# Optimization experiments

Hardware: AMD Instinct MI355X
Metric: run time of the kernel (lower is better)

Reference implementation:

```python
import jax, jax.numpy as jnp
import numpy as np

NEG_SLOPE = 0.2  # PyG GATConv default leaky_relu slope


def _gat_layer(h, mask, W, att_src, att_dst, bias, concat):
    """PyG-style GATConv (eval mode, add_self_loops handled via mask diag).
    h: [B,N,D_in], mask: [B,N,N] bool (mask[b,i,j]=True if edge j->i, incl. self loop)
    W: [D_in, H*C], att_src/att_dst: [H,C], bias: [H*C] or [C].
    """
    B, N, _ = h.shape
    H, C = att_src.shape
    x = (h @ W).reshape(B, N, H, C)                       # [B,N,H,C]
    e_src = jnp.einsum('bnhc,hc->bnh', x, att_src)        # score contrib of source j
    e_dst = jnp.einsum('bnhc,hc->bnh', x, att_dst)        # score contrib of target i
    # scores[b,i,j,h] = leaky_relu(e_dst_i + e_src_j)
    s = jax.nn.leaky_relu(e_dst[:, :, None, :] + e_src[:, None, :, :], NEG_SLOPE)
    s = jnp.where(mask[..., None], s, -jnp.inf)
    alpha = jax.nn.softmax(s, axis=2)                     # softmax over neighbors j
    out = jnp.einsum('bijh,bjhc->bihc', alpha, x)         # aggregate
    out = out.reshape(B, N, H * C) if concat else out.mean(axis=2)
    return out + bias


def setup_inputs() -> dict:
    key = jax.random.key(0)
    ks = jax.random.split(key, 16)
    B, T, N, F_in = 4, 8, 2000, 158
    D, H = 128, 4
    C = D // H  # 32
    x_alpha = jax.random.normal(ks[0], (B, T, N, F_in), dtype=jnp.float32)
    sector_graph = (jax.random.uniform(ks[1], (B, N, N)) > 0.98).astype(jnp.float32)
    g = lambda k, shp, fan: jax.random.normal(k, shp, dtype=jnp.float32) / np.sqrt(fan)
    return {
        'x_alpha': x_alpha,
        'sector_graph': sector_graph,
        'W_in': g(ks[2], (F_in, D), F_in), 'b_in': jnp.zeros((D,), jnp.float32),
        'ln_g': jnp.ones((D,), jnp.float32), 'ln_b': jnp.zeros((D,), jnp.float32),
        'W0': g(ks[3], (D, H * C), D), 'as0': g(ks[4], (H, C), C), 'ad0': g(ks[5], (H, C), C),
        'bias0': jnp.zeros((H * C,), jnp.float32),
        'W1': g(ks[6], (D, H * C), D), 'as1': g(ks[7], (H, C), C), 'ad1': g(ks[8], (H, C), C),
        'bias1': jnp.zeros((C,), jnp.float32),
        'W_out': g(ks[9], (C, D), C), 'b_out': jnp.zeros((D,), jnp.float32),
    }


def reference(x_alpha, sector_graph, W_in, b_in, ln_g, ln_b,
              W0, as0, ad0, bias0, W1, as1, ad1, bias1, W_out, b_out):
    B, T, N, _ = x_alpha.shape
    x = x_alpha[:, -1]                                    # [B,N,F]
    # input_proj: Linear -> LayerNorm -> ReLU (dropout is identity in eval)
    h = x @ W_in + b_in
    mu = h.mean(-1, keepdims=True)
    var = ((h - mu) ** 2).mean(-1, keepdims=True)
    h = (h - mu) / jnp.sqrt(var + 1e-5) * ln_g + ln_b
    h = jax.nn.relu(h)                                    # [B,N,128]
    # edge mask with self loops (PyG add_self_loops=True)
    eye = jnp.eye(N, dtype=bool)
    mask = (sector_graph > 0) | eye[None]
    # layer 0: concat=True, out dim 128 == in dim -> residual, elu (not last layer)
    h0 = _gat_layer(h, mask, W0, as0, ad0, bias0, concat=True)
    h = h + jax.nn.elu(h0)
    # layer 1 (last): concat=False, out dim 32 != 128 -> no residual, no elu
    h = _gat_layer(h, mask, W1, as1, ad1, bias1, concat=False)  # [B,N,32]
    return h @ W_out + b_out                              # [B,N,128]
```

## Files before the change

kernel.cpp:

```cpp
#include <hip/hip_runtime.h>

typedef unsigned short u16;

__device__ __forceinline__ float us2f(u16 u){
  unsigned int x = ((unsigned int)u) << 16;
  return __uint_as_float(x);
}
__device__ __forceinline__ u16 f2us(float f){
  unsigned int u = __float_as_uint(f);
  unsigned int r = (u + 0x7fffu + ((u >> 16) & 1u)) >> 16;
  return (u16)r;
}
__device__ __forceinline__ float wredSum(float v){
  #pragma unroll
  for (int o = 32; o > 0; o >>= 1) v += __shfl_xor(v, o, 64);
  return v;
}
__device__ __forceinline__ float g32Sum(float v){
  #pragma unroll
  for (int o = 16; o > 0; o >>= 1) v += __shfl_xor(v, o, 32);
  return v;
}
__device__ __forceinline__ float g8Sum(float v){
  #pragma unroll
  for (int o = 4; o > 0; o >>= 1) v += __shfl_xor(v, o, 32);
  return v;
}

#define ACAP 128
#define RB 32

__global__ __launch_bounds__(256) void k_adj(
    const float* __restrict__ sg, u16* __restrict__ adj, int* __restrict__ cnt)
{
  __shared__ int c_s;
  const int t = threadIdx.x;
  const int bi = blockIdx.x;
  const int b = bi / 2000;
  const int i = bi - b * 2000;
  if (t == 0) c_s = 0;
  __syncthreads();
  if (t < 250){
    const float4* row4 = (const float4*)(sg + (size_t)bi * 2000);
    float4 v0 = row4[t * 2], v1 = row4[t * 2 + 1];
    const float vv[8] = { v0.x, v0.y, v0.z, v0.w, v1.x, v1.y, v1.z, v1.w };
    int loc[8], nl = 0;
    const int j0 = t * 8;
    #pragma unroll
    for (int q = 0; q < 8; q++){
      int j = j0 + q;
      if (vv[q] > 0.f || j == i) loc[nl++] = j;
    }
    if (nl){
      int p = atomicAdd(&c_s, nl);
      for (int q = 0; q < nl; q++)
        if (p + q < ACAP) adj[(size_t)bi * ACAP + p + q] = (u16)loc[q];
    }
  }
  __syncthreads();
  if (t == 0) cnt[bi] = min(c_s, ACAP);
}

__global__ __launch_bounds__(256) void k_inln_gat0(
    const float* __restrict__ xA, const float* __restrict__ Win,
    const float* __restrict__ bin, const float* __restrict__ lng,
    const float* __restrict__ lnb, const float* __restrict__ W0,
    const float* __restrict__ as0, const float* __restrict__ ad0,
    float* __restrict__ h, u16* __restrict__ x0,
    float* __restrict__ es, float* __restrict__ ed)
{
  __shared__ float xs[RB][160];
  __shared__ float Wt[2][8][128];
  const int t = threadIdx.x;
  const int row0 = blockIdx.x * RB;
  const int tx = t & 31, ty = t >> 5;
  const int c0 = tx * 4, rbase = ty * 4;
  const int wk = ty;

  for (int idx = t; idx < RB * 160; idx += 256){
    int r = idx / 160, k = idx - r * 160;
    int row = row0 + r;
    int b = row / 2000, n = row - b * 2000;
    xs[r][k] = (k < 158) ? xA[(((size_t)b * 8 + 7) * 2000 + n) * 158 + k] : 0.f;
  }
  *(float4*)&Wt[0][wk][c0] = *(const float4*)&Win[(size_t)wk * 128 + c0];
  __syncthreads();

  float acc[4][4];
  #pragma unroll
  for (int r = 0; r < 4; r++)
    #pragma unroll
    for (int c = 0; c < 4; c++) acc[r][c] = 0.f;

  const int NT1 = 20;
  for (int tl = 0; tl < NT1; tl++){
    const int cur = tl & 1;
    float4 wreg = make_float4(0.f, 0.f, 0.f, 0.f);
    const bool hn = (tl + 1 < NT1);
    if (hn){
      int k = (tl + 1) * 8 + wk;
      if (k < 158) wreg = *(const float4*)&Win[(size_t)k * 128 + c0];
    }
    const int k0 = tl * 8;
    #pragma unroll
    for (int kh = 0; kh < 2; kh++){
      float4 a[4];
      #pragma unroll
      for (int r = 0; r < 4; r++) a[r] = *(const float4*)&xs[rbase + r][k0 + kh * 4];
      #pragma unroll
      for (int kk = 0; kk < 4; kk++){
        float4 w = *(const float4*)&Wt[cur][kh * 4 + kk][c0];
        #pragma unroll
        for (int r = 0; r < 4; r++){
          float av = ((const float*)&a[r])[kk];
          acc[r][0] = fmaf(av, w.x, acc[r][0]);
          acc[r][1] = fmaf(av, w.y, acc[r][1]);
          acc[r][2] = fmaf(av, w.z, acc[r][2]);
          acc[r][3] = fmaf(av, w.w, acc[r][3]);
        }
      }
    }
    if (hn) *(float4*)&Wt[cur ^ 1][wk][c0] = wreg;
    __syncthreads();
  }

  {
    float4 bi = *(const float4*)&bin[c0];
    float4 g  = *(const float4*)&lng[c0];
    float4 be = *(const float4*)&lnb[c0];
    #pragma unroll
    for (int r = 0; r < 4; r++){
      float a0 = acc[r][0] + bi.x, a1 = acc[r][1] + bi.y;
      float a2 = acc[r][2] + bi.z, a3 = acc[r][3] + bi.w;
      float s  = g32Sum(a0 + a1 + a2 + a3);
      float sq = g32Sum(a0*a0 + a1*a1 + a2*a2 + a3*a3);
      float mu  = s * (1.f / 128.f);
      float var = sq * (1.f / 128.f) - mu * mu;
      float inv = rsqrtf(var + 1e-5f);
      float v0 = fmaxf((a0 - mu) * inv * g.x + be.x, 0.f);
      float v1 = fmaxf((a1 - mu) * inv * g.y + be.y, 0.f);
      float v2 = fmaxf((a2 - mu) * inv * g.z + be.z, 0.f);
      float v3 = fmaxf((a3 - mu) * inv * g.w + be.w, 0.f);
      *(float4*)&xs[rbase + r][c0] = make_float4(v0, v1, v2, v3);
      *(float4*)&h[(size_t)(row0 + rbase + r) * 128 + c0] = make_float4(v0, v1, v2, v3);
    }
  }
  *(float4*)&Wt[0][wk][c0] = *(const float4*)&W0[(size_t)wk * 128 + c0];
  __syncthreads();

  #pragma unroll
  for (int r = 0; r < 4; r++)
    #pragma unroll
    for (int c = 0; c < 4; c++) acc[r][c] = 0.f;
  const int NT2 = 16;
  for (int tl = 0; tl < NT2; tl++){
    const int cur = tl & 1;
    float4 wreg = make_float4(0.f, 0.f, 0.f, 0.f);
    const bool hn = (tl + 1 < NT2);
    if (hn) wreg = *(const float4*)&W0[(size_t)((tl + 1) * 8 + wk) * 128 + c0];
    const int k0 = tl * 8;
    #pragma unroll
    for (int kh = 0; kh < 2; kh++){
      float4 a[4];
      #pragma unroll
      for (int r = 0; r < 4; r++) a[r] = *(const float4*)&xs[rbase + r][k0 + kh * 4];
      #pragma unroll
      for (int kk = 0; kk < 4; kk++){
        float4 w = *(const float4*)&Wt[cur][kh * 4 + kk][c0];
        #pragma unroll
        for (int r = 0; r < 4; r++){
          float av = ((const float*)&a[r])[kk];
          acc[r][0] = fmaf(av, w.x, acc[r][0]);
          acc[r][1] = fmaf(av, w.y, acc[r][1]);
          acc[r][2] = fmaf(av, w.z, acc[r][2]);
          acc[r][3] = fmaf(av, w.w, acc[r][3]);
        }
      }
    }
    if (hn) *(float4*)&Wt[cur ^ 1][wk][c0] = wreg;
    __syncthreads();
  }

  {
    float4 av = *(const float4*)&as0[c0];
    float4 dv = *(const float4*)&ad0[c0];
    const int hh = tx >> 3;
    #pragma unroll
    for (int r = 0; r < 4; r++){
      ushort4 o;
      o.x = f2us(acc[r][0]); o.y = f2us(acc[r][1]);
      o.z = f2us(acc[r][2]); o.w = f2us(acc[r][3]);
      *(ushort4*)(x0 + (size_t)(row0 + rbase + r) * 128 + c0) = o;
      float ps = acc[r][0]*av.x + acc[r][1]*av.y + acc[r][2]*av.z + acc[r][3]*av.w;
      float pd = acc[r][0]*dv.x + acc[r][1]*dv.y + acc[r][2]*dv.z + acc[r][3]*dv.w;
      ps = g8Sum(ps); pd = g8Sum(pd);
      if ((tx & 7) == 0){
        es[(size_t)(row0 + rbase + r) * 4 + hh] = ps;
        ed[(size_t)(row0 + rbase + r) * 4 + hh] = pd;
      }
    }
  }
}

__global__ __launch_bounds__(256) void k_gat_pre(
    const float* __restrict__ hin, const float* __restrict__ W,
    const float* __restrict__ asv, const float* __restrict__ adv,
    u16* __restrict__ x0, float* __restrict__ es, float* __restrict__ ed)
{
  __shared__ float xs[RB][128];
  __shared__ float Wt[2][8][128];
  const int t = threadIdx.x;
  const int row0 = blockIdx.x * RB;
  const int tx = t & 31, ty = t >> 5;
  const int c0 = tx * 4, rbase = ty * 4;
  const int wk = ty;

  for (int f = t; f < RB * 32; f += 256){
    int r = f >> 5, cq = (f & 31) * 4;
    *(float4*)&xs[r][cq] = *(const float4*)&hin[(size_t)(row0 + r) * 128 + cq];
  }
  *(float4*)&Wt[0][wk][c0] = *(const float4*)&W[(size_t)wk * 128 + c0];
  __syncthreads();

  float acc[4][4];
  #pragma unroll
  for (int r = 0; r < 4; r++)
    #pragma unroll
    for (int c = 0; c < 4; c++) acc[r][c] = 0.f;

  const int NT = 16;
  for (int tl = 0; tl < NT; tl++){
    const int cur = tl & 1;
    float4 wreg = make_float4(0.f, 0.f, 0.f, 0.f);
    const bool hn = (tl + 1 < NT);
    if (hn) wreg = *(const float4*)&W[(size_t)((tl + 1) * 8 + wk) * 128 + c0];
    const int k0 = tl * 8;
    #pragma unroll
    for (int kh = 0; kh < 2; kh++){
      float4 a[4];
      #pragma unroll
      for (int r = 0; r < 4; r++) a[r] = *(const float4*)&xs[rbase + r][k0 + kh * 4];
      #pragma unroll
      for (int kk = 0; kk < 4; kk++){
        float4 w = *(const float4*)&Wt[cur][kh * 4 + kk][c0];
        #pragma unroll
        for (int r = 0; r < 4; r++){
          float av = ((const float*)&a[r])[kk];
          acc[r][0] = fmaf(av, w.x, acc[r][0]);
          acc[r][1] = fmaf(av, w.y, acc[r][1]);
          acc[r][2] = fmaf(av, w.z, acc[r][2]);
          acc[r][3] = fmaf(av, w.w, acc[r][3]);
        }
      }
    }
    if (hn) *(float4*)&Wt[cur ^ 1][wk][c0] = wreg;
    __syncthreads();
  }

  {
    float4 av = *(const float4*)&asv[c0];
    float4 dv = *(const float4*)&adv[c0];
    const int hh = tx >> 3;
    #pragma unroll
    for (int r = 0; r < 4; r++){
      ushort4 o;
      o.x = f2us(acc[r][0]); o.y = f2us(acc[r][1]);
      o.z = f2us(acc[r][2]); o.w = f2us(acc[r][3]);
      *(ushort4*)(x0 + (size_t)(row0 + rbase + r) * 128 + c0) = o;
      float ps = acc[r][0]*av.x + acc[r][1]*av.y + acc[r][2]*av.z + acc[r][3]*av.w;
      float pd = acc[r][0]*dv.x + acc[r][1]*dv.y + acc[r][2]*dv.z + acc[r][3]*dv.w;
      ps = g8Sum(ps); pd = g8Sum(pd);
      if ((tx & 7) == 0){
        es[(size_t)(row0 + rbase + r) * 4 + hh] = ps;
        ed[(size_t)(row0 + rbase + r) * 4 + hh] = pd;
      }
    }
  }
}

template<int LAYER>
__global__ __launch_bounds__(128) void k_attn(
    const u16* __restrict__ adj, const int* __restrict__ cnt,
    const u16* __restrict__ x0,
    const float* __restrict__ es, const float* __restrict__ ed,
    const float* __restrict__ bias, float* __restrict__ hio,
    const float* __restrict__ Wout, const float* __restrict__ bout,
    float* __restrict__ outv)
{
  __shared__ int idx_s[ACAP];
  __shared__ float sc[4][ACAP];
  __shared__ float red[2][4];
  __shared__ float Ssh[4];
  __shared__ float r128[128];
  __shared__ float mrow[32];
  const int t = threadIdx.x;
  const int bi = blockIdx.x;
  const int b = bi / 2000;

  const int m = min(cnt[bi], ACAP);

  float4 edv = *(const float4*)&ed[(size_t)bi * 4];
  float p0 = 0.f, p1 = 0.f, p2 = 0.f, p3 = 0.f;
  if (t < m){
    int j = (int)adj[(size_t)bi * ACAP + t];
    idx_s[t] = j;
    float4 esv = *(const float4*)&es[((size_t)b * 2000 + j) * 4];
    float s0 = edv.x + esv.x; s0 = s0 > 0.f ? s0 : 0.2f * s0;
    float s1 = edv.y + esv.y; s1 = s1 > 0.f ? s1 : 0.2f * s1;
    float s2 = edv.z + esv.z; s2 = s2 > 0.f ? s2 : 0.2f * s2;
    float s3 = edv.w + esv.w; s3 = s3 > 0.f ? s3 : 0.2f * s3;
    p0 = __expf(s0); p1 = __expf(s1); p2 = __expf(s2); p3 = __expf(s3);
    sc[0][t] = p0; sc[1][t] = p1; sc[2][t] = p2; sc[3][t] = p3;
  }
  float q0 = wredSum(p0), q1 = wredSum(p1), q2 = wredSum(p2), q3 = wredSum(p3);
  if ((t & 63) == 0){ int w = t >> 6; red[w][0] = q0; red[w][1] = q1; red[w][2] = q2; red[w][3] = q3; }
  __syncthreads();
  if (t < 4) Ssh[t] = red[0][t] + red[1][t];
  __syncthreads();

  const int hh = t >> 5;
  float acc = 0.f;
  const u16* x0b = x0 + (size_t)b * 2000 * 128 + t;
  #pragma unroll 8
  for (int e = 0; e < m; e++){
    int j2 = idx_s[e];
    acc = fmaf(sc[hh][e], us2f(x0b[(size_t)j2 * 128]), acc);
  }
  acc /= Ssh[hh];

  if (LAYER == 0){
    float v = acc + bias[t];
    v = v > 0.f ? v : (__expf(v) - 1.f);
    hio[(size_t)bi * 128 + t] += v;
  } else {
    r128[t] = acc;
    __syncthreads();
    if (t < 32)
      mrow[t] = (r128[t] + r128[t + 32] + r128[t + 64] + r128[t + 96]) * 0.25f + bias[t];
    __syncthreads();
    float o = bout[t];
    #pragma unroll
    for (int k = 0; k < 32; k++) o = fmaf(mrow[k], Wout[(size_t)k * 128 + t], o);
    outv[(size_t)bi * 128 + t] = o;
  }
}

extern "C" void kernel_launch(void* const* d_in, const int* in_sizes, int n_in,
                              void* d_out, int out_size, void* d_ws, size_t ws_size,
                              hipStream_t stream) {
  const float* xA   = (const float*)d_in[0];
  const float* sg   = (const float*)d_in[1];
  const float* Win  = (const float*)d_in[2];
  const float* bin  = (const float*)d_in[3];
  const float* lng  = (const float*)d_in[4];
  const float* lnb  = (const float*)d_in[5];
  const float* W0   = (const float*)d_in[6];
  const float* as0  = (const float*)d_in[7];
  const float* ad0  = (const float*)d_in[8];
  const float* b0   = (const float*)d_in[9];
  const float* W1   = (const float*)d_in[10];
  const float* as1  = (const float*)d_in[11];
  const float* ad1  = (const float*)d_in[12];
  const float* b1   = (const float*)d_in[13];
  const float* Wout = (const float*)d_in[14];
  const float* bout = (const float*)d_in[15];

  char* ws = (char*)d_ws;
  float* h    = (float*)(ws);
  u16*   x0   = (u16*)  (ws + 4096000);
  float* es   = (float*)(ws + 6144000);
  float* ed   = (float*)(ws + 6272000);
  u16*   adj  = (u16*)  (ws + 6400000);
  int*   cnt  = (int*)  (ws + 8448000);

  k_adj       <<<8000, 256, 0, stream>>>(sg, adj, cnt);
  k_inln_gat0 <<<250, 256, 0, stream>>>(xA, Win, bin, lng, lnb, W0, as0, ad0, h, x0, es, ed);
  k_attn<0>   <<<8000, 128, 0, stream>>>(adj, cnt, x0, es, ed, b0, h, nullptr, nullptr, nullptr);
  k_gat_pre   <<<250, 256, 0, stream>>>(h, W1, as1, ad1, x0, es, ed);
  k_attn<1>   <<<8000, 128, 0, stream>>>(adj, cnt, x0, es, ed, b1, nullptr, Wout, bout, (float*)d_out);
}
```

Before: 212.7 us.

## Fuse adjacency build into layer-0 attention, use wave-per-row attention, halve GEMM row blocks

Removes the separate adjacency-extraction kernel and builds each row's neighbor list inside the layer-0 attention kernel, one 64-lane wave per target node with four nodes per block. Each lane now handles two channels using packed 32-bit bf16 loads. The layer-1 head-mean and output projection use shuffles instead of shared memory and barriers. The projection kernels drop to 16-row blocks, doubling the grid size for better occupancy at the cost of less weight reuse. The in-kernel adjacency build uses per-element shared atomics, and the attention kernel now carries extra shared memory.

```diff
diff --git a/kernel.cpp b/kernel.cpp
--- a/kernel.cpp
+++ b/kernel.cpp
@@ -28,38 +28,7 @@
 }
 
 #define ACAP 128
-#define RB 32
-
-__global__ __launch_bounds__(256) void k_adj(
-    const float* __restrict__ sg, u16* __restrict__ adj, int* __restrict__ cnt)
-{
-  __shared__ int c_s;
-  const int t = threadIdx.x;
-  const int bi = blockIdx.x;
-  const int b = bi / 2000;
-  const int i = bi - b * 2000;
-  if (t == 0) c_s = 0;
-  __syncthreads();
-  if (t < 250){
-    const float4* row4 = (const float4*)(sg + (size_t)bi * 2000);
-    float4 v0 = row4[t * 2], v1 = row4[t * 2 + 1];
-    const float vv[8] = { v0.x, v0.y, v0.z, v0.w, v1.x, v1.y, v1.z, v1.w };
-    int loc[8], nl = 0;
-    const int j0 = t * 8;
-    #pragma unroll
-    for (int q = 0; q < 8; q++){
-      int j = j0 + q;
-      if (vv[q] > 0.f || j == i) loc[nl++] = j;
-    }
-    if (nl){
-      int p = atomicAdd(&c_s, nl);
-      for (int q = 0; q < nl; q++)
-        if (p + q < ACAP) adj[(size_t)bi * ACAP + p + q] = (u16)loc[q];
-    }
-  }
-  __syncthreads();
-  if (t == 0) cnt[bi] = min(c_s, ACAP);
-}
+#define RB 16
 
 __global__ __launch_bounds__(256) void k_inln_gat0(
     const float* __restrict__ xA, const float* __restrict__ Win,
@@ -74,21 +43,22 @@
   const int t = threadIdx.x;
   const int row0 = blockIdx.x * RB;
   const int tx = t & 31, ty = t >> 5;
-  const int c0 = tx * 4, rbase = ty * 4;
+  const int c0 = tx * 4, rbase = ty * 2;
   const int wk = ty;
+  const int b = row0 / 2000;
+  const int n0 = row0 - b * 2000;
+  const size_t xbase = (((size_t)b * 8 + 7) * 2000 + n0) * 158;
 
   for (int idx = t; idx < RB * 160; idx += 256){
     int r = idx / 160, k = idx - r * 160;
-    int row = row0 + r;
-    int b = row / 2000, n = row - b * 2000;
-    xs[r][k] = (k < 158) ? xA[(((size_t)b * 8 + 7) * 2000 + n) * 158 + k] : 0.f;
+    xs[r][k] = (k < 158) ? xA[xbase + (size_t)r * 158 + k] : 0.f;
   }
   *(float4*)&Wt[0][wk][c0] = *(const float4*)&Win[(size_t)wk * 128 + c0];
   __syncthreads();
 
-  float acc[4][4];
-  #pragma unroll
-  for (int r = 0; r < 4; r++)
+  float acc[2][4];
+  #pragma unroll
+  for (int r = 0; r < 2; r++)
     #pragma unroll
     for (int c = 0; c < 4; c++) acc[r][c] = 0.f;
 
@@ -104,14 +74,14 @@
     const int k0 = tl * 8;
     #pragma unroll
     for (int kh = 0; kh < 2; kh++){
-      float4 a[4];
-      #pragma unroll
-      for (int r = 0; r < 4; r++) a[r] = *(const float4*)&xs[rbase + r][k0 + kh * 4];
+      float4 a[2];
+      #pragma unroll
+      for (int r = 0; r < 2; r++) a[r] = *(const float4*)&xs[rbase + r][k0 + kh * 4];
       #pragma unroll
       for (int kk = 0; kk < 4; kk++){
         float4 w = *(const float4*)&Wt[cur][kh * 4 + kk][c0];
         #pragma unroll
-        for (int r = 0; r < 4; r++){
+        for (int r = 0; r < 2; r++){
           float av = ((const float*)&a[r])[kk];
           acc[r][0] = fmaf(av, w.x, acc[r][0]);
           acc[r][1] = fmaf(av, w.y, acc[r][1]);
@@ -129,7 +99,7 @@
     float4 g  = *(const float4*)&lng[c0];
     float4 be = *(const float4*)&lnb[c0];
     #pragma unroll
-    for (int r = 0; r < 4; r++){
+    for (int r = 0; r < 2; r++){
       float a0 = acc[r][0] + bi.x, a1 = acc[r][1] + bi.y;
       float a2 = acc[r][2] + bi.z, a3 = acc[r][3] + bi.w;
       float s  = g32Sum(a0 + a1 + a2 + a3);
@@ -149,7 +119,7 @@
   __syncthreads();
 
   #pragma unroll
-  for (int r = 0; r < 4; r++)
+  for (int r = 0; r < 2; r++)
     #pragma unroll
     for (int c = 0; c < 4; c++) acc[r][c] = 0.f;
   const int NT2 = 16;
@@ -161,14 +131,14 @@
     const int k0 = tl * 8;
     #pragma unroll
     for (int kh = 0; kh < 2; kh++){
-      float4 a[4];
-      #pragma unroll
-      for (int r = 0; r < 4; r++) a[r] = *(const float4*)&xs[rbase + r][k0 + kh * 4];
+      float4 a[2];
+      #pragma unroll
+      for (int r = 0; r < 2; r++) a[r] = *(const float4*)&xs[rbase + r][k0 + kh * 4];
       #pragma unroll
       for (int kk = 0; kk < 4; kk++){
         float4 w = *(const float4*)&Wt[cur][kh * 4 + kk][c0];
         #pragma unroll
-        for (int r = 0; r < 4; r++){
+        for (int r = 0; r < 2; r++){
           float av = ((const float*)&a[r])[kk];
           acc[r][0] = fmaf(av, w.x, acc[r][0]);
           acc[r][1] = fmaf(av, w.y, acc[r][1]);
@@ -186,7 +156,7 @@
     float4 dv = *(const float4*)&ad0[c0];
     const int hh = tx >> 3;
     #pragma unroll
-    for (int r = 0; r < 4; r++){
+    for (int r = 0; r < 2; r++){
       ushort4 o;
       o.x = f2us(acc[r][0]); o.y = f2us(acc[r][1]);
       o.z = f2us(acc[r][2]); o.w = f2us(acc[r][3]);
@@ -212,7 +182,7 @@
   const int t = threadIdx.x;
   const int row0 = blockIdx.x * RB;
   const int tx = t & 31, ty = t >> 5;
-  const int c0 = tx * 4, rbase = ty * 4;
+  const int c0 = tx * 4, rbase = ty * 2;
   const int wk = ty;
 
   for (int f = t; f < RB * 32; f += 256){
@@ -222,9 +192,9 @@
   *(float4*)&Wt[0][wk][c0] = *(const float4*)&W[(size_t)wk * 128 + c0];
   __syncthreads();
 
-  float acc[4][4];
-  #pragma unroll
-  for (int r = 0; r < 4; r++)
+  float acc[2][4];
+  #pragma unroll
+  for (int r = 0; r < 2; r++)
     #pragma unroll
     for (int c = 0; c < 4; c++) acc[r][c] = 0.f;
 
@@ -237,14 +207,14 @@
     const int k0 = tl * 8;
     #pragma unroll
     for (int kh = 0; kh < 2; kh++){
-      float4 a[4];
-      #pragma unroll
-      for (int r = 0; r < 4; r++) a[r] = *(const float4*)&xs[rbase + r][k0 + kh * 4];
+      float4 a[2];
+      #pragma unroll
+      for (int r = 0; r < 2; r++) a[r] = *(const float4*)&xs[rbase + r][k0 + kh * 4];
       #pragma unroll
       for (int kk = 0; kk < 4; kk++){
         float4 w = *(const float4*)&Wt[cur][kh * 4 + kk][c0];
         #pragma unroll
-        for (int r = 0; r < 4; r++){
+        for (int r = 0; r < 2; r++){
           float av = ((const float*)&a[r])[kk];
           acc[r][0] = fmaf(av, w.x, acc[r][0]);
           acc[r][1] = fmaf(av, w.y, acc[r][1]);
@@ -262,7 +232,7 @@
     float4 dv = *(const float4*)&adv[c0];
     const int hh = tx >> 3;
     #pragma unroll
-    for (int r = 0; r < 4; r++){
+    for (int r = 0; r < 2; r++){
       ushort4 o;
       o.x = f2us(acc[r][0]); o.y = f2us(acc[r][1]);
       o.z = f2us(acc[r][2]); o.w = f2us(acc[r][3]);
@@ -279,69 +249,120 @@
 }
 
 template<int LAYER>
-__global__ __launch_bounds__(128) void k_attn(
-    const u16* __restrict__ adj, const int* __restrict__ cnt,
+__global__ __launch_bounds__(256) void k_attn(
+    const float* __restrict__ sg,
+    u16* __restrict__ adj, int* __restrict__ cnt,
     const u16* __restrict__ x0,
     const float* __restrict__ es, const float* __restrict__ ed,
     const float* __restrict__ bias, float* __restrict__ hio,
     const float* __restrict__ Wout, const float* __restrict__ bout,
     float* __restrict__ outv)
 {
-  __shared__ int idx_s[ACAP];
-  __shared__ float sc[4][ACAP];
-  __shared__ float red[2][4];
-  __shared__ float Ssh[4];
-  __shared__ float r128[128];
-  __shared__ float mrow[32];
+  __shared__ int   idx_s[4][ACAP];
+  __shared__ float sc[4][4][132];
+  __shared__ int   cnt_s[4];
   const int t = threadIdx.x;
-  const int bi = blockIdx.x;
+  const int w = t >> 6;
+  const int l = t & 63;
+  const int bi = blockIdx.x * 4 + w;
   const int b = bi / 2000;
-
-  const int m = min(cnt[bi], ACAP);
+  const int i = bi - b * 2000;
+
+  if (LAYER == 0){
+    if (l == 0) cnt_s[w] = 0;
+    const float4* row4 = (const float4*)(sg + (size_t)bi * 2000);
+    #pragma unroll
+    for (int q = 0; q < 8; q++){
+      int f4 = q * 64 + l;
+      if (f4 < 500){
+        float4 v = row4[f4];
+        int j0 = f4 * 4;
+        #pragma unroll
+        for (int u = 0; u < 4; u++){
+          int j = j0 + u;
+          float vv = (&v.x)[u];
+          if (vv > 0.f || j == i){
+            int p = atomicAdd(&cnt_s[w], 1);
+            if (p < ACAP){
+              idx_s[w][p] = j;
+              adj[(size_t)bi * ACAP + p] = (u16)j;
+            }
+          }
+        }
+      }
+    }
+    if (l == 0) cnt[bi] = min(cnt_s[w], ACAP);
+  } else {
+    int mg = cnt[bi];
+    if (l == 0) cnt_s[w] = mg;
+    if (l < mg)      idx_s[w][l]      = (int)adj[(size_t)bi * ACAP + l];
+    if (64 + l < mg) idx_s[w][64 + l] = (int)adj[(size_t)bi * ACAP + 64 + l];
+  }
+  __syncthreads();
+  const int m = min(cnt_s[w], ACAP);
 
   float4 edv = *(const float4*)&ed[(size_t)bi * 4];
-  float p0 = 0.f, p1 = 0.f, p2 = 0.f, p3 = 0.f;
-  if (t < m){
-    int j = (int)adj[(size_t)bi * ACAP + t];
-    idx_s[t] = j;
-    float4 esv = *(const float4*)&es[((size_t)b * 2000 + j) * 4];
-    float s0 = edv.x + esv.x; s0 = s0 > 0.f ? s0 : 0.2f * s0;
-    float s1 = edv.y + esv.y; s1 = s1 > 0.f ? s1 : 0.2f * s1;
-    float s2 = edv.z + esv.z; s2 = s2 > 0.f ? s2 : 0.2f * s2;
-    float s3 = edv.w + esv.w; s3 = s3 > 0.f ? s3 : 0.2f * s3;
-    p0 = __expf(s0); p1 = __expf(s1); p2 = __expf(s2); p3 = __expf(s3);
-    sc[0][t] = p0; sc[1][t] = p1; sc[2][t] = p2; sc[3][t] = p3;
-  }
-  float q0 = wredSum(p0), q1 = wredSum(p1), q2 = wredSum(p2), q3 = wredSum(p3);
-  if ((t & 63) == 0){ int w = t >> 6; red[w][0] = q0; red[w][1] = q1; red[w][2] = q2; red[w][3] = q3; }
+  float q0 = 0.f, q1 = 0.f, q2 = 0.f, q3 = 0.f;
+  #pragma unroll
+  for (int rep = 0; rep < 2; rep++){
+    int e = rep * 64 + l;
+    if (e < m){
+      int j = idx_s[w][e];
+      float4 esv = *(const float4*)&es[((size_t)b * 2000 + j) * 4];
+      float s0 = edv.x + esv.x; s0 = s0 > 0.f ? s0 : 0.2f * s0;
+      float s1 = edv.y + esv.y; s1 = s1 > 0.f ? s1 : 0.2f * s1;
+      float s2 = edv.z + esv.z; s2 = s2 > 0.f ? s2 : 0.2f * s2;
+      float s3 = edv.w + esv.w; s3 = s3 > 0.f ? s3 : 0.2f * s3;
+      float p0 = __expf(s0), p1 = __expf(s1), p2 = __expf(s2), p3 = __expf(s3);
+      sc[w][0][e] = p0; sc[w][1][e] = p1; sc[w][2][e] = p2; sc[w][3][e] = p3;
+      q0 += p0; q1 += p1; q2 += p2; q3 += p3;
+    }
+  }
+  q0 = wredSum(q0); q1 = wredSum(q1); q2 = wredSum(q2); q3 = wredSum(q3);
   __syncthreads();
-  if (t < 4) Ssh[t] = red[0][t] + red[1][t];
-  __syncthreads();
-
-  const int hh = t >> 5;
-  float acc = 0.f;
-  const u16* x0b = x0 + (size_t)b * 2000 * 128 + t;
+
+  const int hh = l >> 4;
+  float qh = hh < 2 ? (hh == 0 ? q0 : q1) : (hh == 2 ? q2 : q3);
+  float inv = 1.f / qh;
+  float a0 = 0.f, a1 = 0.f;
+  const u16* x0b = x0 + (size_t)b * 2000 * 128 + 2 * l;
   #pragma unroll 8
   for (int e = 0; e < m; e++){
-    int j2 = idx_s[e];
-    acc = fmaf(sc[hh][e], us2f(x0b[(size_t)j2 * 128]), acc);
-  }
-  acc /= Ssh[hh];
+    float p = sc[w][hh][e];
+    int j = idx_s[w][e];
+    unsigned int pk = *(const unsigned int*)(x0b + (size_t)j * 128);
+    a0 = fmaf(p, us2f((u16)(pk & 0xffffu)), a0);
+    a1 = fmaf(p, us2f((u16)(pk >> 16)), a1);
+  }
+  a0 *= inv; a1 *= inv;
 
   if (LAYER == 0){
-    float v = acc + bias[t];
-    v = v > 0.f ? v : (__expf(v) - 1.f);
-    hio[(size_t)bi * 128 + t] += v;
+    float2 bb = *(const float2*)&bias[2 * l];
+    float v0 = a0 + bb.x; v0 = v0 > 0.f ? v0 : (__expf(v0) - 1.f);
+    float v1 = a1 + bb.y; v1 = v1 > 0.f ? v1 : (__expf(v1) - 1.f);
+    float2* hp = (float2*)&hio[(size_t)bi * 128 + 2 * l];
+    float2 ho = *hp;
+    *hp = make_float2(ho.x + v0, ho.y + v1);
   } else {
-    r128[t] = acc;
-    __syncthreads();
-    if (t < 32)
-      mrow[t] = (r128[t] + r128[t + 32] + r128[t + 64] + r128[t + 96]) * 0.25f + bias[t];
-    __syncthreads();
-    float o = bout[t];
-    #pragma unroll
-    for (int k = 0; k < 32; k++) o = fmaf(mrow[k], Wout[(size_t)k * 128 + t], o);
-    outv[(size_t)bi * 128 + t] = o;
+    float s0 = a0 + __shfl_xor(a0, 16); s0 += __shfl_xor(s0, 32);
+    float s1 = a1 + __shfl_xor(a1, 16); s1 += __shfl_xor(s1, 32);
+    float mv0 = s0 * 0.25f, mv1 = s1 * 0.25f;
+    if (l < 16){
+      float2 bb = *(const float2*)&bias[2 * l];
+      mv0 += bb.x; mv1 += bb.y;
+    }
+    float2 bo = *(const float2*)&bout[2 * l];
+    float o0 = bo.x, o1 = bo.y;
+    #pragma unroll
+    for (int p = 0; p < 16; p++){
+      float mk0 = __shfl(mv0, p);
+      float mk1 = __shfl(mv1, p);
+      float2 w0 = *(const float2*)&Wout[(size_t)(2 * p) * 128 + 2 * l];
+      float2 w1 = *(const float2*)&Wout[(size_t)(2 * p + 1) * 128 + 2 * l];
+      o0 = fmaf(mk0, w0.x, o0); o1 = fmaf(mk0, w0.y, o1);
+      o0 = fmaf(mk1, w1.x, o0); o1 = fmaf(mk1, w1.y, o1);
+    }
+    *(float2*)&outv[(size_t)bi * 128 + 2 * l] = make_float2(o0, o1);
   }
 }
 
@@ -373,9 +394,8 @@
   u16*   adj  = (u16*)  (ws + 6400000);
   int*   cnt  = (int*)  (ws + 8448000);
 
-  k_adj       <<<8000, 256, 0, stream>>>(sg, adj, cnt);
-  k_inln_gat0 <<<250, 256, 0, stream>>>(xA, Win, bin, lng, lnb, W0, as0, ad0, h, x0, es, ed);
-  k_attn<0>   <<<8000, 128, 0, stream>>>(adj, cnt, x0, es, ed, b0, h, nullptr, nullptr, nullptr);
-  k_gat_pre   <<<250, 256, 0, stream>>>(h, W1, as1, ad1, x0, es, ed);
-  k_attn<1>   <<<8000, 128, 0, stream>>>(adj, cnt, x0, es, ed, b1, nullptr, Wout, bout, (float*)d_out);
-}
+  k_inln_gat0 <<<500, 256, 0, stream>>>(xA, Win, bin, lng, lnb, W0, as0, ad0, h, x0, es, ed);
+  k_attn<0>   <<<2000, 256, 0, stream>>>(sg, adj, cnt, x0, es, ed, b0, h, nullptr, nullptr, nullptr);
+  k_gat_pre   <<<500, 256, 0, stream>>>(h, W1, as1, ad1, x0, es, ed);
+  k_attn<1>   <<<2000, 256, 0, stream>>>(nullptr, adj, cnt, x0, es, ed, b1, nullptr, Wout, bout, (float*)d_out);
+}
```

Result: faster. 200.5 us (median of 2 runs) (-5.7%).
